# Optimization experiments

Hardware: AMD Instinct MI355X
Metric: run time of the kernel (lower is better)

Reference implementation:

```python
import jax, jax.numpy as jnp
import numpy as np

N = 100000   # nodes ('paper')
E = 500000   # edges per etype
ET = 3       # edge types
L = 2        # GAT layers
F = 256      # in_feats == h_feats
H = 4        # heads
D = 64       # head dim = h_feats // n_heads
C = 349      # num_classes
NEG_SLOPE = 0.2


def setup_inputs() -> dict:
    key = jax.random.key(0)
    ks = jax.random.split(key, 10)
    x = jax.random.normal(ks[0], (N, F), jnp.float32)
    # stacked per-(layer, etype) GATConv params
    W = jax.random.normal(ks[1], (L, ET, F, H * D), jnp.float32) * 0.05
    attn_l = jax.random.normal(ks[2], (L, ET, H, D), jnp.float32) * 0.1
    attn_r = jax.random.normal(ks[3], (L, ET, H, D), jnp.float32) * 0.1
    bias = jnp.zeros((L, ET, H * D), jnp.float32)
    W_out = jax.random.normal(ks[4], (H * D, C), jnp.float32) * 0.05
    b_out = jnp.zeros((C,), jnp.float32)
    src = jax.random.randint(ks[5], (ET, E), 0, N, dtype=jnp.int32)
    dst = jax.random.randint(ks[6], (ET, E), 0, N, dtype=jnp.int32)
    return {"x": x, "W": W, "attn_l": attn_l, "attn_r": attn_r, "bias": bias,
            "W_out": W_out, "b_out": b_out, "src": src, "dst": dst}


def _gat_etype(h, W_le, al, ar, b, s, d):
    # h: [N,F] -> feat: [N,H,D]
    feat = (h @ W_le).reshape(-1, H, D)
    el = jnp.einsum('nhd,hd->nh', feat, al)   # [N,H]
    er = jnp.einsum('nhd,hd->nh', feat, ar)   # [N,H]
    logits = jax.nn.leaky_relu(el[s] + er[d], NEG_SLOPE)  # [E,H]
    # segment softmax over incoming edges of each dst node
    m = jax.ops.segment_max(logits, d, num_segments=N)     # [N,H]
    a = jnp.exp(logits - m[d])                              # [E,H]
    denom = jax.ops.segment_sum(a, d, num_segments=N)      # [N,H]
    alpha = a / denom[d]                                    # [E,H]
    msg = alpha[:, :, None] * feat[s]                       # [E,H,D]
    agg = jax.ops.segment_sum(msg, d, num_segments=N)      # [N,H,D]
    return agg + b.reshape(H, D)


def reference(x, W, attn_l, attn_r, bias, W_out, b_out, src, dst):
    h = x
    for l in range(L):
        out = jnp.zeros((N, H, D), x.dtype)
        for e in range(ET):  # HeteroGraphConv default 'sum' aggregation
            out = out + _gat_etype(h, W[l, e], attn_l[l, e], attn_r[l, e],
                                   bias[l, e], src[e], dst[e])
        h = out.reshape(N, H * D)  # concat heads (view)
        if l != L - 1:
            h = jax.nn.relu(h)  # dropout is identity in eval mode
    return h @ W_out + b_out
```

## Files before the change

kernel.cpp:

```cpp
#include <hip/hip_runtime.h>
#include <hip/hip_fp16.h>

#define N_NODES 100000
#define N_EDGES 500000
#define M_PAD   100096
#define NCHUNK  196

using f32x4  = __attribute__((ext_vector_type(4))) float;
using bf16x8 = __attribute__((ext_vector_type(8))) __bf16;

__device__ __forceinline__ ushort f2bf(float f) {
  union { float f; unsigned u; } v; v.f = f;
  unsigned r = v.u + 0x7fffu + ((v.u >> 16) & 1u);
  return (ushort)(r >> 16);
}
__device__ __forceinline__ float bf2f(ushort b) {
  union { unsigned u; float f; } v; v.u = ((unsigned)b) << 16;
  return v.f;
}

__global__ __launch_bounds__(256) void cvt_x_kernel(const float* __restrict__ x,
                                                    ushort* __restrict__ h) {
  const size_t i = (size_t)blockIdx.x * 256 + threadIdx.x;
  ushort4 o;
  if (i < (size_t)N_NODES * 64) {
    const float4 v = ((const float4*)x)[i];
    o.x = f2bf(v.x); o.y = f2bf(v.y); o.z = f2bf(v.z); o.w = f2bf(v.w);
  } else {
    o.x = 0; o.y = 0; o.z = 0; o.w = 0;
  }
  ((ushort4*)h)[i] = o;
}

__global__ __launch_bounds__(256) void cvt_w_kernel(const float* __restrict__ W,
                                                    ushort* __restrict__ Wt) {
  const int i = blockIdx.x * 256 + threadIdx.x;
  const int le = i >> 16, r = i & 65535, nn = r >> 8, kk = r & 255;
  Wt[i] = f2bf(W[(le << 16) | (kk << 8) | nn]);
}

__global__ __launch_bounds__(256) void cvt_wout_kernel(const float* __restrict__ Wo,
                                                       ushort* __restrict__ Wto) {
  const int i = blockIdx.x * 256 + threadIdx.x;
  const int nn = i >> 8, kk = i & 255;
  Wto[i] = f2bf(nn < 349 ? Wo[kk * 349 + nn] : 0.f);
}

__global__ __launch_bounds__(256) void zero_cnt_kernel(int* __restrict__ cnt) {
  const int i = blockIdx.x * 256 + threadIdx.x;
  if (i < 3 * N_NODES) cnt[i] = 0;
}

__global__ __launch_bounds__(256) void hist_kernel(const int* __restrict__ dst,
                                                   int* __restrict__ cnt) {
  const int i = blockIdx.x * 256 + threadIdx.x;
  if (i >= 3 * N_EDGES) return;
  const int et = i / N_EDGES;
  atomicAdd(&cnt[et * N_NODES + dst[i]], 1);
}

__global__ __launch_bounds__(512) void scan1_kernel(const int* __restrict__ cnt,
                                                    int* __restrict__ rowp,
                                                    int* __restrict__ bsum) {
  __shared__ int sm[512];
  const int et = blockIdx.y, c = blockIdx.x, tid = threadIdx.x;
  const int idx = c * 512 + tid;
  const int v = (idx < N_NODES) ? cnt[et * N_NODES + idx] : 0;
  sm[tid] = v; __syncthreads();
  for (int off = 1; off < 512; off <<= 1) {
    const int tmp = (tid >= off) ? sm[tid - off] : 0;
    __syncthreads();
    sm[tid] += tmp;
    __syncthreads();
  }
  if (idx < N_NODES) rowp[et * (N_NODES + 1) + idx] = sm[tid] - v;
  if (tid == 511) bsum[et * NCHUNK + c] = sm[511];
}

__global__ __launch_bounds__(256) void scan2_kernel(int* __restrict__ bsum) {
  __shared__ int sm[256];
  const int et = blockIdx.x, tid = threadIdx.x;
  const int v = (tid < NCHUNK) ? bsum[et * NCHUNK + tid] : 0;
  sm[tid] = v; __syncthreads();
  for (int off = 1; off < 256; off <<= 1) {
    const int tmp = (tid >= off) ? sm[tid - off] : 0;
    __syncthreads();
    sm[tid] += tmp;
    __syncthreads();
  }
  if (tid < NCHUNK) bsum[et * NCHUNK + tid] = sm[tid] - v;
}

__global__ __launch_bounds__(512) void scan3_kernel(int* __restrict__ rowp,
                                                    const int* __restrict__ bsum,
                                                    int* __restrict__ cur) {
  const int et = blockIdx.y, c = blockIdx.x, tid = threadIdx.x;
  const int idx = c * 512 + tid;
  if (idx < N_NODES) {
    const int v = rowp[et * (N_NODES + 1) + idx] + bsum[et * NCHUNK + c];
    rowp[et * (N_NODES + 1) + idx] = v;
    cur[et * N_NODES + idx] = v;
  }
  if (c == 0 && tid == 0) rowp[et * (N_NODES + 1) + N_NODES] = N_EDGES;
}

__global__ __launch_bounds__(256) void scatter_kernel(const int* __restrict__ src,
                                                      const int* __restrict__ dst,
                                                      int* __restrict__ cur,
                                                      int* __restrict__ perm,
                                                      int* __restrict__ dstc) {
  const int i = blockIdx.x * 256 + threadIdx.x;
  if (i >= 3 * N_EDGES) return;
  const int et = i / N_EDGES;
  const int d = dst[i];
  const int pos = atomicAdd(&cur[et * N_NODES + d], 1);
  perm[et * N_EDGES + pos] = src[i];
  dstc[et * N_EDGES + pos] = d;
}

__global__ __launch_bounds__(256, 2) void gemm_feat_fused(
    const ushort* __restrict__ A, const ushort* __restrict__ WtL,
    ushort* __restrict__ feat, const float* __restrict__ attn_l,
    const float* __restrict__ attn_r, float* __restrict__ el,
    float* __restrict__ er, int layer) {
  __shared__ ushort As[128 * 64];
  __shared__ ushort Bs[3 * 128 * 64];
  const int t = threadIdx.x;
  const int lane = t & 63;
  const int wave = t >> 6;
  const int wm = (wave >> 1) << 6;
  const int wn = (wave & 1) << 6;
  const int quad = lane >> 4;
  const int ln = lane & 15;
  const size_t m0 = (size_t)blockIdx.x * 128;
  const size_t n0 = (size_t)blockIdx.y * 128;

  f32x4 acc[3][4][4];
#pragma unroll
  for (int e = 0; e < 3; ++e)
#pragma unroll
    for (int x = 0; x < 4; ++x)
#pragma unroll
      for (int y = 0; y < 4; ++y)
        acc[e][x][y] = (f32x4){0.f, 0.f, 0.f, 0.f};

  for (int k0 = 0; k0 < 256; k0 += 64) {
    __syncthreads();
#pragma unroll
    for (int i = 0; i < 4; ++i) {
      const int f = i * 256 + t;
      const int row = f >> 3;
      const int cl = (f & 7) ^ (row & 7);
      const int ldsbase = (i * 256 + (t & ~63)) << 3;
      __builtin_amdgcn_global_load_lds(
          (const __attribute__((address_space(1))) void*)(A + (m0 + row) * 256 + k0 + cl * 8),
          (__attribute__((address_space(3))) void*)(As + ldsbase), 16, 0, 0);
#pragma unroll
      for (int e = 0; e < 3; ++e)
        __builtin_amdgcn_global_load_lds(
            (const __attribute__((address_space(1))) void*)(WtL + (e << 16) + (n0 + row) * 256 + k0 + cl * 8),
            (__attribute__((address_space(3))) void*)(Bs + e * 8192 + ldsbase), 16, 0, 0);
    }
    __syncthreads();
#pragma unroll
    for (int s = 0; s < 2; ++s) {
      const int cl = s * 4 + quad;
      bf16x8 af[4];
#pragma unroll
      for (int x = 0; x < 4; ++x) {
        const int mm = wm + x * 16 + ln;
        af[x] = *(const bf16x8*)(As + mm * 64 + ((cl ^ (mm & 7)) << 3));
      }
#pragma unroll
      for (int e = 0; e < 3; ++e) {
        bf16x8 bfr[4];
#pragma unroll
        for (int y = 0; y < 4; ++y) {
          const int nn = wn + y * 16 + ln;
          bfr[y] = *(const bf16x8*)(Bs + e * 8192 + nn * 64 + ((cl ^ (nn & 7)) << 3));
        }
#pragma unroll
        for (int x = 0; x < 4; ++x)
#pragma unroll
          for (int y = 0; y < 4; ++y)
            acc[e][x][y] = __builtin_amdgcn_mfma_f32_16x16x32_bf16(bfr[y], af[x], acc[e][x][y], 0, 0, 0);
      }
    }
  }

  const int h = (int)(n0 + wn) >> 6;
#pragma unroll
  for (int e = 0; e < 3; ++e) {
    ushort* C = feat + (size_t)e * M_PAD * 256;
#pragma unroll
    for (int x = 0; x < 4; ++x) {
      const size_t m = m0 + wm + x * 16 + ln;
#pragma unroll
      for (int y = 0; y < 4; ++y) {
        const size_t n = n0 + wn + y * 16 + quad * 4;
        ushort4 o;
        o.x = f2bf(acc[e][x][y][0]); o.y = f2bf(acc[e][x][y][1]);
        o.z = f2bf(acc[e][x][y][2]); o.w = f2bf(acc[e][x][y][3]);
        *(ushort4*)(C + m * 256 + n) = o;
      }
    }
    const float* al = attn_l + (((layer * 3 + e) * 4 + h) << 6);
    const float* ar = attn_r + (((layer * 3 + e) * 4 + h) << 6);
    float4 alv[4], arv[4];
#pragma unroll
    for (int y = 0; y < 4; ++y) {
      alv[y] = *(const float4*)(al + y * 16 + quad * 4);
      arv[y] = *(const float4*)(ar + y * 16 + quad * 4);
    }
#pragma unroll
    for (int x = 0; x < 4; ++x) {
      float pl = 0.f, pr = 0.f;
#pragma unroll
      for (int y = 0; y < 4; ++y) {
        pl += acc[e][x][y][0] * alv[y].x + acc[e][x][y][1] * alv[y].y +
              acc[e][x][y][2] * alv[y].z + acc[e][x][y][3] * alv[y].w;
        pr += acc[e][x][y][0] * arv[y].x + acc[e][x][y][1] * arv[y].y +
              acc[e][x][y][2] * arv[y].z + acc[e][x][y][3] * arv[y].w;
      }
      pl += __shfl_xor(pl, 16); pl += __shfl_xor(pl, 32);
      pr += __shfl_xor(pr, 16); pr += __shfl_xor(pr, 32);
      const int m = (int)m0 + wm + x * 16 + ln;
      if (quad == 0 && m < N_NODES) {
        el[((size_t)e * N_NODES + m) * 4 + h] = pl;
        er[((size_t)e * N_NODES + m) * 4 + h] = pr;
      }
    }
  }
}

__global__ __launch_bounds__(256) void gemm128(const ushort* __restrict__ A,
                                               const ushort* __restrict__ Bt,
                                               float* __restrict__ C,
                                               const float* __restrict__ obias,
                                               int ldc, int nmax, int mmax) {
  __shared__ ushort As[128 * 64];
  __shared__ ushort Bs[128 * 64];
  const int t = threadIdx.x;
  const int lane = t & 63;
  const int wave = t >> 6;
  const int wm = (wave >> 1) << 6;
  const int wn = (wave & 1) << 6;
  const int quad = lane >> 4;
  const int ln = lane & 15;
  const size_t m0 = (size_t)blockIdx.x * 128;
  const size_t n0 = (size_t)blockIdx.y * 128;

  f32x4 acc[4][4];
#pragma unroll
  for (int x = 0; x < 4; ++x)
#pragma unroll
    for (int y = 0; y < 4; ++y)
      acc[x][y] = (f32x4){0.f, 0.f, 0.f, 0.f};

  for (int k0 = 0; k0 < 256; k0 += 64) {
    __syncthreads();
#pragma unroll
    for (int i = 0; i < 4; ++i) {
      const int f = i * 256 + t;
      const int row = f >> 3;
      const int cl = (f & 7) ^ (row & 7);
      const int ldsbase = (i * 256 + (t & ~63)) << 3;
      __builtin_amdgcn_global_load_lds(
          (const __attribute__((address_space(1))) void*)(A + (m0 + row) * 256 + k0 + cl * 8),
          (__attribute__((address_space(3))) void*)(As + ldsbase), 16, 0, 0);
      __builtin_amdgcn_global_load_lds(
          (const __attribute__((address_space(1))) void*)(Bt + (n0 + row) * 256 + k0 + cl * 8),
          (__attribute__((address_space(3))) void*)(Bs + ldsbase), 16, 0, 0);
    }
    __syncthreads();
#pragma unroll
    for (int s = 0; s < 2; ++s) {
      bf16x8 af[4], bfr[4];
      const int cl = s * 4 + quad;
#pragma unroll
      for (int x = 0; x < 4; ++x) {
        const int mm = wm + x * 16 + ln;
        af[x] = *(const bf16x8*)(As + mm * 64 + ((cl ^ (mm & 7)) << 3));
        const int nn = wn + x * 16 + ln;
        bfr[x] = *(const bf16x8*)(Bs + nn * 64 + ((cl ^ (nn & 7)) << 3));
      }
#pragma unroll
      for (int x = 0; x < 4; ++x)
#pragma unroll
        for (int y = 0; y < 4; ++y)
          acc[x][y] = __builtin_amdgcn_mfma_f32_16x16x32_bf16(bfr[y], af[x], acc[x][y], 0, 0, 0);
    }
  }

#pragma unroll
  for (int x = 0; x < 4; ++x) {
    const int m = (int)m0 + wm + x * 16 + ln;
    if (m < mmax) {
#pragma unroll
      for (int y = 0; y < 4; ++y) {
        const int n = (int)n0 + wn + y * 16 + quad * 4;
#pragma unroll
        for (int r = 0; r < 4; ++r)
          if (n + r < nmax)
            C[(size_t)m * ldc + n + r] = acc[x][y][r] + obias[n + r];
      }
    }
  }
}

__global__ __launch_bounds__(256) void wcalc_kernel(const int* __restrict__ perm,
                                                    const int* __restrict__ dstc,
                                                    const float* __restrict__ el,
                                                    const float* __restrict__ er,
                                                    ushort* __restrict__ wcsr) {
  const int i = blockIdx.x * 256 + threadIdx.x;
  if (i >= 3 * N_EDGES) return;
  const int et = i / N_EDGES;
  const int s = perm[i];
  const int d = dstc[i];
  const float4 l4 = ((const float4*)el)[(size_t)et * N_NODES + s];
  const float4 r4 = ((const float4*)er)[(size_t)et * N_NODES + d];
  float z0 = l4.x + r4.x, z1 = l4.y + r4.y, z2 = l4.z + r4.z, z3 = l4.w + r4.w;
  z0 = (z0 > 0.f) ? z0 : 0.2f * z0;
  z1 = (z1 > 0.f) ? z1 : 0.2f * z1;
  z2 = (z2 > 0.f) ? z2 : 0.2f * z2;
  z3 = (z3 > 0.f) ? z3 : 0.2f * z3;
  ushort4 o;
  o.x = __half_as_ushort(__float2half(__expf(z0)));
  o.y = __half_as_ushort(__float2half(__expf(z1)));
  o.z = __half_as_ushort(__float2half(__expf(z2)));
  o.w = __half_as_ushort(__float2half(__expf(z3)));
  ((ushort4*)wcsr)[i] = o;
}

__global__ __launch_bounds__(256) void agg_kernel(const ushort* __restrict__ feat,
                                                  const ushort* __restrict__ wcsr,
                                                  const int* __restrict__ rowp,
                                                  const int* __restrict__ perm,
                                                  const float* __restrict__ bias,
                                                  ushort* __restrict__ hout,
                                                  int layer, int do_relu) {
  const int wave = threadIdx.x >> 6, lane = threadIdx.x & 63;
  const int n = blockIdx.x * 4 + wave;
  const int h = lane >> 4;
  const float* bl = bias + layer * 768 + (lane << 2);
  float a0 = bl[0] + bl[256] + bl[512];
  float a1 = bl[1] + bl[257] + bl[513];
  float a2 = bl[2] + bl[258] + bl[514];
  float a3 = bl[3] + bl[259] + bl[515];
#pragma unroll
  for (int et = 0; et < 3; ++et) {
    const int beg = rowp[et * (N_NODES + 1) + n];
    const int end = rowp[et * (N_NODES + 1) + n + 1];
    if (end == beg) continue;
    const int* ps = perm + (size_t)et * N_EDGES;
    const ushort* wc = wcsr + (size_t)et * N_EDGES * 4;
    const ushort* fb = feat + (size_t)et * M_PAD * 256;
    const int last = end - 1;
    float l0 = 0.f, l1 = 0.f, l2 = 0.f, l3 = 0.f, den = 0.f;
    for (int i = beg; i < end; i += 8) {
      int idx[8];
#pragma unroll
      for (int j = 0; j < 8; ++j)
        idx[j] = (i + j < last) ? (i + j) : last;
      int sj[8];
#pragma unroll
      for (int j = 0; j < 8; ++j)
        sj[j] = ps[idx[j]];
      float wj[8];
#pragma unroll
      for (int j = 0; j < 8; ++j) {
        const float t = __half2float(__ushort_as_half(wc[idx[j] * 4 + h]));
        wj[j] = (i + j <= last) ? t : 0.f;
      }
      ushort4 fv[8];
#pragma unroll
      for (int j = 0; j < 8; ++j)
        fv[j] = *(const ushort4*)(fb + (size_t)sj[j] * 256 + (lane << 2));
#pragma unroll
      for (int j = 0; j < 8; ++j) {
        den += wj[j];
        l0 += wj[j] * bf2f(fv[j].x); l1 += wj[j] * bf2f(fv[j].y);
        l2 += wj[j] * bf2f(fv[j].z); l3 += wj[j] * bf2f(fv[j].w);
      }
    }
    const float inv = 1.0f / den;
    a0 += l0 * inv; a1 += l1 * inv; a2 += l2 * inv; a3 += l3 * inv;
  }
  if (do_relu) {
    a0 = fmaxf(a0, 0.f); a1 = fmaxf(a1, 0.f);
    a2 = fmaxf(a2, 0.f); a3 = fmaxf(a3, 0.f);
  }
  ushort4 o;
  o.x = f2bf(a0); o.y = f2bf(a1); o.z = f2bf(a2); o.w = f2bf(a3);
  *(ushort4*)(hout + (size_t)n * 256 + (lane << 2)) = o;
}

extern "C" void kernel_launch(void* const* d_in, const int* in_sizes, int n_in,
                              void* d_out, int out_size, void* d_ws, size_t ws_size,
                              hipStream_t stream) {
  const float* x      = (const float*)d_in[0];
  const float* W      = (const float*)d_in[1];
  const float* attn_l = (const float*)d_in[2];
  const float* attn_r = (const float*)d_in[3];
  const float* bias   = (const float*)d_in[4];
  const float* W_out  = (const float*)d_in[5];
  const float* b_out  = (const float*)d_in[6];
  const int*   src    = (const int*)d_in[7];
  const int*   dst    = (const int*)d_in[8];

  char* p = (char*)d_ws;
  auto carve = [&](size_t bytes) {
    char* r = p;
    p += (bytes + 255) & ~(size_t)255;
    return r;
  };
  ushort* h_bf  = (ushort*)carve((size_t)M_PAD * 256 * 2);
  ushort* feat  = (ushort*)carve((size_t)3 * M_PAD * 256 * 2);
  ushort* Wt    = (ushort*)carve((size_t)6 * 65536 * 2);
  ushort* Wto   = (ushort*)carve((size_t)384 * 256 * 2);
  float*  el    = (float*)carve((size_t)3 * N_NODES * 4 * 4);
  float*  er    = (float*)carve((size_t)3 * N_NODES * 4 * 4);
  int*    cnt   = (int*)carve((size_t)3 * N_NODES * 4);
  int*    rowp  = (int*)carve((size_t)3 * (N_NODES + 1) * 4);
  int*    cur   = (int*)carve((size_t)3 * N_NODES * 4);
  int*    perm  = (int*)carve((size_t)3 * N_EDGES * 4);
  int*    dstc  = (int*)carve((size_t)3 * N_EDGES * 4);
  ushort* wcsr  = (ushort*)carve((size_t)3 * N_EDGES * 4 * 2);
  int*    bsum  = (int*)carve((size_t)3 * NCHUNK * 4);

  cvt_x_kernel<<<M_PAD * 64 / 256, 256, 0, stream>>>(x, h_bf);
  cvt_w_kernel<<<6 * 65536 / 256, 256, 0, stream>>>(W, Wt);
  cvt_wout_kernel<<<384 * 256 / 256, 256, 0, stream>>>(W_out, Wto);

  zero_cnt_kernel<<<(3 * N_NODES + 255) / 256, 256, 0, stream>>>(cnt);
  hist_kernel<<<(3 * N_EDGES + 255) / 256, 256, 0, stream>>>(dst, cnt);
  scan1_kernel<<<dim3(NCHUNK, 3), 512, 0, stream>>>(cnt, rowp, bsum);
  scan2_kernel<<<3, 256, 0, stream>>>(bsum);
  scan3_kernel<<<dim3(NCHUNK, 3), 512, 0, stream>>>(rowp, bsum, cur);
  scatter_kernel<<<(3 * N_EDGES + 255) / 256, 256, 0, stream>>>(src, dst, cur, perm, dstc);

  for (int l = 0; l < 2; ++l) {
    gemm_feat_fused<<<dim3(M_PAD / 128, 2), 256, 0, stream>>>(
        h_bf, Wt + (size_t)l * 3 * 65536, feat, attn_l, attn_r, el, er, l);
    wcalc_kernel<<<(3 * N_EDGES + 255) / 256, 256, 0, stream>>>(perm, dstc, el, er, wcsr);
    agg_kernel<<<N_NODES / 4, 256, 0, stream>>>(feat, wcsr, rowp, perm, bias,
                                                h_bf, l, l == 0 ? 1 : 0);
  }
  gemm128<<<dim3(M_PAD / 128, 3), 256, 0, stream>>>(h_bf, Wto, (float*)d_out,
                                                    b_out, 349, 349, N_NODES);
}
```

Measured before the change: 980.8 us.

## Merge per-etype CSRs into one dst CSR with prenormalized attention weights

Builds a single CSR over all three edge types keyed by destination. Each edge stores global src/dst ids offset by etype*M_PAD. Softmax denominators are computed by atomic adds in wcalc, inverted, and folded into the fp16 weights by a new normalization pass, so aggregation visits each node's edges in one loop with no per-etype divide. The aggregation kernel also becomes a grid-stride loop over 2048 blocks. This adds several extra kernels and float atomics per layer, and normalizing in fp16 changes rounding.

```diff
diff --git a/kernel.cpp b/kernel.cpp
--- a/kernel.cpp
+++ b/kernel.cpp
@@ -5,6 +5,7 @@
 #define N_EDGES 500000
 #define M_PAD   100096
 #define NCHUNK  196
+#define DEN_ELEMS (3 * M_PAD * 4)
 
 using f32x4  = __attribute__((ext_vector_type(4))) float;
 using bf16x8 = __attribute__((ext_vector_type(8))) __bf16;
@@ -48,24 +49,23 @@
 
 __global__ __launch_bounds__(256) void zero_cnt_kernel(int* __restrict__ cnt) {
   const int i = blockIdx.x * 256 + threadIdx.x;
-  if (i < 3 * N_NODES) cnt[i] = 0;
+  if (i < N_NODES) cnt[i] = 0;
 }
 
 __global__ __launch_bounds__(256) void hist_kernel(const int* __restrict__ dst,
                                                    int* __restrict__ cnt) {
   const int i = blockIdx.x * 256 + threadIdx.x;
   if (i >= 3 * N_EDGES) return;
-  const int et = i / N_EDGES;
-  atomicAdd(&cnt[et * N_NODES + dst[i]], 1);
+  atomicAdd(&cnt[dst[i]], 1);
 }
 
 __global__ __launch_bounds__(512) void scan1_kernel(const int* __restrict__ cnt,
                                                     int* __restrict__ rowp,
                                                     int* __restrict__ bsum) {
   __shared__ int sm[512];
-  const int et = blockIdx.y, c = blockIdx.x, tid = threadIdx.x;
+  const int c = blockIdx.x, tid = threadIdx.x;
   const int idx = c * 512 + tid;
-  const int v = (idx < N_NODES) ? cnt[et * N_NODES + idx] : 0;
+  const int v = (idx < N_NODES) ? cnt[idx] : 0;
   sm[tid] = v; __syncthreads();
   for (int off = 1; off < 512; off <<= 1) {
     const int tmp = (tid >= off) ? sm[tid - off] : 0;
@@ -73,14 +73,14 @@
     sm[tid] += tmp;
     __syncthreads();
   }
-  if (idx < N_NODES) rowp[et * (N_NODES + 1) + idx] = sm[tid] - v;
-  if (tid == 511) bsum[et * NCHUNK + c] = sm[511];
+  if (idx < N_NODES) rowp[idx] = sm[tid] - v;
+  if (tid == 511) bsum[c] = sm[511];
 }
 
 __global__ __launch_bounds__(256) void scan2_kernel(int* __restrict__ bsum) {
   __shared__ int sm[256];
-  const int et = blockIdx.x, tid = threadIdx.x;
-  const int v = (tid < NCHUNK) ? bsum[et * NCHUNK + tid] : 0;
+  const int tid = threadIdx.x;
+  const int v = (tid < NCHUNK) ? bsum[tid] : 0;
   sm[tid] = v; __syncthreads();
   for (int off = 1; off < 256; off <<= 1) {
     const int tmp = (tid >= off) ? sm[tid - off] : 0;
@@ -88,34 +88,34 @@
     sm[tid] += tmp;
     __syncthreads();
   }
-  if (tid < NCHUNK) bsum[et * NCHUNK + tid] = sm[tid] - v;
+  if (tid < NCHUNK) bsum[tid] = sm[tid] - v;
 }
 
 __global__ __launch_bounds__(512) void scan3_kernel(int* __restrict__ rowp,
                                                     const int* __restrict__ bsum,
                                                     int* __restrict__ cur) {
-  const int et = blockIdx.y, c = blockIdx.x, tid = threadIdx.x;
+  const int c = blockIdx.x, tid = threadIdx.x;
   const int idx = c * 512 + tid;
   if (idx < N_NODES) {
-    const int v = rowp[et * (N_NODES + 1) + idx] + bsum[et * NCHUNK + c];
-    rowp[et * (N_NODES + 1) + idx] = v;
-    cur[et * N_NODES + idx] = v;
-  }
-  if (c == 0 && tid == 0) rowp[et * (N_NODES + 1) + N_NODES] = N_EDGES;
+    const int v = rowp[idx] + bsum[c];
+    rowp[idx] = v;
+    cur[idx] = v;
+  }
+  if (c == 0 && tid == 0) rowp[N_NODES] = 3 * N_EDGES;
 }
 
 __global__ __launch_bounds__(256) void scatter_kernel(const int* __restrict__ src,
                                                       const int* __restrict__ dst,
                                                       int* __restrict__ cur,
-                                                      int* __restrict__ perm,
-                                                      int* __restrict__ dstc) {
+                                                      uint* __restrict__ srcid,
+                                                      uint* __restrict__ dstid) {
   const int i = blockIdx.x * 256 + threadIdx.x;
   if (i >= 3 * N_EDGES) return;
   const int et = i / N_EDGES;
   const int d = dst[i];
-  const int pos = atomicAdd(&cur[et * N_NODES + d], 1);
-  perm[et * N_EDGES + pos] = src[i];
-  dstc[et * N_EDGES + pos] = d;
+  const int pos = atomicAdd(&cur[d], 1);
+  srcid[pos] = (uint)(et * M_PAD + src[i]);
+  dstid[pos] = (uint)(et * M_PAD + d);
 }
 
 __global__ __launch_bounds__(256, 2) void gemm_feat_fused(
@@ -226,8 +226,8 @@
       pr += __shfl_xor(pr, 16); pr += __shfl_xor(pr, 32);
       const int m = (int)m0 + wm + x * 16 + ln;
       if (quad == 0 && m < N_NODES) {
-        el[((size_t)e * N_NODES + m) * 4 + h] = pl;
-        er[((size_t)e * N_NODES + m) * 4 + h] = pr;
+        el[((size_t)e * M_PAD + m) * 4 + h] = pl;
+        er[((size_t)e * M_PAD + m) * 4 + h] = pr;
       }
     }
   }
@@ -308,92 +308,132 @@
   }
 }
 
-__global__ __launch_bounds__(256) void wcalc_kernel(const int* __restrict__ perm,
-                                                    const int* __restrict__ dstc,
+__global__ __launch_bounds__(256) void wcalc_kernel(const uint* __restrict__ srcid,
+                                                    const uint* __restrict__ dstid,
                                                     const float* __restrict__ el,
                                                     const float* __restrict__ er,
-                                                    ushort* __restrict__ wcsr) {
+                                                    ushort* __restrict__ wcsr,
+                                                    float* __restrict__ den) {
   const int i = blockIdx.x * 256 + threadIdx.x;
   if (i >= 3 * N_EDGES) return;
-  const int et = i / N_EDGES;
-  const int s = perm[i];
-  const int d = dstc[i];
-  const float4 l4 = ((const float4*)el)[(size_t)et * N_NODES + s];
-  const float4 r4 = ((const float4*)er)[(size_t)et * N_NODES + d];
+  const uint sid = srcid[i];
+  const uint did = dstid[i];
+  const float4 l4 = ((const float4*)el)[sid];
+  const float4 r4 = ((const float4*)er)[did];
   float z0 = l4.x + r4.x, z1 = l4.y + r4.y, z2 = l4.z + r4.z, z3 = l4.w + r4.w;
   z0 = (z0 > 0.f) ? z0 : 0.2f * z0;
   z1 = (z1 > 0.f) ? z1 : 0.2f * z1;
   z2 = (z2 > 0.f) ? z2 : 0.2f * z2;
   z3 = (z3 > 0.f) ? z3 : 0.2f * z3;
+  const float w0 = __expf(z0), w1 = __expf(z1), w2 = __expf(z2), w3 = __expf(z3);
   ushort4 o;
-  o.x = __half_as_ushort(__float2half(__expf(z0)));
-  o.y = __half_as_ushort(__float2half(__expf(z1)));
-  o.z = __half_as_ushort(__float2half(__expf(z2)));
-  o.w = __half_as_ushort(__float2half(__expf(z3)));
+  o.x = __half_as_ushort(__float2half(w0));
+  o.y = __half_as_ushort(__float2half(w1));
+  o.z = __half_as_ushort(__float2half(w2));
+  o.w = __half_as_ushort(__float2half(w3));
+  ((ushort4*)wcsr)[i] = o;
+  float* dp = den + (size_t)did * 4;
+  atomicAdd(dp + 0, w0); atomicAdd(dp + 1, w1);
+  atomicAdd(dp + 2, w2); atomicAdd(dp + 3, w3);
+}
+
+__global__ __launch_bounds__(256) void zero_den_kernel(float* __restrict__ den) {
+  const int i = blockIdx.x * 256 + threadIdx.x;
+  if (i < DEN_ELEMS) den[i] = 0.f;
+}
+
+__global__ __launch_bounds__(256) void rcp_den_kernel(float* __restrict__ den) {
+  const int i = blockIdx.x * 256 + threadIdx.x;
+  if (i < DEN_ELEMS) {
+    const float d = den[i];
+    den[i] = (d != 0.f) ? __builtin_amdgcn_rcpf(d) : 0.f;
+  }
+}
+
+__global__ __launch_bounds__(256) void wnorm_kernel(const uint* __restrict__ dstid,
+                                                    const float* __restrict__ rden,
+                                                    ushort* __restrict__ wcsr) {
+  const int i = blockIdx.x * 256 + threadIdx.x;
+  if (i >= 3 * N_EDGES) return;
+  const uint did = dstid[i];
+  const float4 r4 = ((const float4*)rden)[did];
+  const ushort4 w = ((const ushort4*)wcsr)[i];
+  ushort4 o;
+  o.x = __half_as_ushort(__float2half(__half2float(__ushort_as_half(w.x)) * r4.x));
+  o.y = __half_as_ushort(__float2half(__half2float(__ushort_as_half(w.y)) * r4.y));
+  o.z = __half_as_ushort(__float2half(__half2float(__ushort_as_half(w.z)) * r4.z));
+  o.w = __half_as_ushort(__float2half(__half2float(__ushort_as_half(w.w)) * r4.w));
   ((ushort4*)wcsr)[i] = o;
 }
 
 __global__ __launch_bounds__(256) void agg_kernel(const ushort* __restrict__ feat,
                                                   const ushort* __restrict__ wcsr,
                                                   const int* __restrict__ rowp,
-                                                  const int* __restrict__ perm,
+                                                  const uint* __restrict__ srcid,
                                                   const float* __restrict__ bias,
                                                   ushort* __restrict__ hout,
                                                   int layer, int do_relu) {
-  const int wave = threadIdx.x >> 6, lane = threadIdx.x & 63;
-  const int n = blockIdx.x * 4 + wave;
-  const int h = lane >> 4;
+  const int wv   = __builtin_amdgcn_readfirstlane((int)(threadIdx.x >> 6));
+  const int lane = threadIdx.x & 63;
+  const int h2   = (lane >> 4) << 1;
+  const int f8   = lane << 3;
   const float* bl = bias + layer * 768 + (lane << 2);
-  float a0 = bl[0] + bl[256] + bl[512];
-  float a1 = bl[1] + bl[257] + bl[513];
-  float a2 = bl[2] + bl[258] + bl[514];
-  float a3 = bl[3] + bl[259] + bl[515];
-#pragma unroll
-  for (int et = 0; et < 3; ++et) {
-    const int beg = rowp[et * (N_NODES + 1) + n];
-    const int end = rowp[et * (N_NODES + 1) + n + 1];
-    if (end == beg) continue;
-    const int* ps = perm + (size_t)et * N_EDGES;
-    const ushort* wc = wcsr + (size_t)et * N_EDGES * 4;
-    const ushort* fb = feat + (size_t)et * M_PAD * 256;
-    const int last = end - 1;
-    float l0 = 0.f, l1 = 0.f, l2 = 0.f, l3 = 0.f, den = 0.f;
-    for (int i = beg; i < end; i += 8) {
-      int idx[8];
-#pragma unroll
-      for (int j = 0; j < 8; ++j)
-        idx[j] = (i + j < last) ? (i + j) : last;
-      int sj[8];
-#pragma unroll
-      for (int j = 0; j < 8; ++j)
-        sj[j] = ps[idx[j]];
-      float wj[8];
-#pragma unroll
-      for (int j = 0; j < 8; ++j) {
-        const float t = __half2float(__ushort_as_half(wc[idx[j] * 4 + h]));
-        wj[j] = (i + j <= last) ? t : 0.f;
-      }
-      ushort4 fv[8];
-#pragma unroll
-      for (int j = 0; j < 8; ++j)
-        fv[j] = *(const ushort4*)(fb + (size_t)sj[j] * 256 + (lane << 2));
-#pragma unroll
-      for (int j = 0; j < 8; ++j) {
-        den += wj[j];
-        l0 += wj[j] * bf2f(fv[j].x); l1 += wj[j] * bf2f(fv[j].y);
-        l2 += wj[j] * bf2f(fv[j].z); l3 += wj[j] * bf2f(fv[j].w);
-      }
-    }
-    const float inv = 1.0f / den;
-    a0 += l0 * inv; a1 += l1 * inv; a2 += l2 * inv; a3 += l3 * inv;
-  }
-  if (do_relu) {
-    a0 = fmaxf(a0, 0.f); a1 = fmaxf(a1, 0.f);
-    a2 = fmaxf(a2, 0.f); a3 = fmaxf(a3, 0.f);
-  }
-  ushort4 o;
-  o.x = f2bf(a0); o.y = f2bf(a1); o.z = f2bf(a2); o.w = f2bf(a3);
-  *(ushort4*)(hout + (size_t)n * 256 + (lane << 2)) = o;
+  const float b0 = bl[0] + bl[256] + bl[512];
+  const float b1 = bl[1] + bl[257] + bl[513];
+  const float b2 = bl[2] + bl[258] + bl[514];
+  const float b3 = bl[3] + bl[259] + bl[515];
+  const char* wb = (const char*)wcsr;
+  const char* fb = (const char*)feat;
+  for (int n = blockIdx.x * 4 + wv; n < N_NODES; n += 8192) {
+    const int beg = rowp[n];
+    const int end = rowp[n + 1];
+    float a0 = b0, a1 = b1, a2 = b2, a3 = b3;
+    if (end > beg) {
+      const int last = end - 1;
+      float l0 = 0.f, l1 = 0.f, l2 = 0.f, l3 = 0.f;
+      for (int i = beg; i < end; i += 8) {
+        int idx[8];
+#pragma unroll
+        for (int j = 0; j < 8; ++j)
+          idx[j] = (i + j < last) ? (i + j) : last;
+        uint sd[8];
+#pragma unroll
+        for (int j = 0; j < 8; ++j)
+          sd[j] = srcid[idx[j]];
+        float wj[8];
+#pragma unroll
+        for (int j = 0; j < 8; ++j) {
+          const ushort wu = *(const ushort*)(wb + ((size_t)idx[j] << 3) + h2);
+          const float t = __half2float(__ushort_as_half(wu));
+          wj[j] = (i + j <= last) ? t : 0.f;
+        }
+        uint2 fv[8];
+#pragma unroll
+        for (int j = 0; j < 8; ++j)
+          fv[j] = *(const uint2*)(fb + ((size_t)sd[j] << 9) + f8);
+#pragma unroll
+        for (int j = 0; j < 8; ++j) {
+          union { uint u; float f; } c0, c1, c2, c3;
+          c0.u = fv[j].x << 16;
+          c1.u = fv[j].x & 0xffff0000u;
+          c2.u = fv[j].y << 16;
+          c3.u = fv[j].y & 0xffff0000u;
+          l0 += wj[j] * c0.f;
+          l1 += wj[j] * c1.f;
+          l2 += wj[j] * c2.f;
+          l3 += wj[j] * c3.f;
+        }
+      }
+      a0 += l0; a1 += l1; a2 += l2; a3 += l3;
+    }
+    if (do_relu) {
+      a0 = fmaxf(a0, 0.f); a1 = fmaxf(a1, 0.f);
+      a2 = fmaxf(a2, 0.f); a3 = fmaxf(a3, 0.f);
+    }
+    ushort4 o;
+    o.x = f2bf(a0); o.y = f2bf(a1); o.z = f2bf(a2); o.w = f2bf(a3);
+    *(ushort4*)(hout + (size_t)n * 256 + (lane << 2)) = o;
+  }
 }
 
 extern "C" void kernel_launch(void* const* d_in, const int* in_sizes, int n_in,
@@ -419,33 +459,37 @@
   ushort* feat  = (ushort*)carve((size_t)3 * M_PAD * 256 * 2);
   ushort* Wt    = (ushort*)carve((size_t)6 * 65536 * 2);
   ushort* Wto   = (ushort*)carve((size_t)384 * 256 * 2);
-  float*  el    = (float*)carve((size_t)3 * N_NODES * 4 * 4);
-  float*  er    = (float*)carve((size_t)3 * N_NODES * 4 * 4);
-  int*    cnt   = (int*)carve((size_t)3 * N_NODES * 4);
-  int*    rowp  = (int*)carve((size_t)3 * (N_NODES + 1) * 4);
-  int*    cur   = (int*)carve((size_t)3 * N_NODES * 4);
-  int*    perm  = (int*)carve((size_t)3 * N_EDGES * 4);
-  int*    dstc  = (int*)carve((size_t)3 * N_EDGES * 4);
+  float*  el    = (float*)carve((size_t)3 * M_PAD * 4 * 4);
+  float*  er    = (float*)carve((size_t)3 * M_PAD * 4 * 4);
+  float*  den   = (float*)carve((size_t)DEN_ELEMS * 4);
+  int*    cnt   = (int*)carve((size_t)N_NODES * 4);
+  int*    rowp  = (int*)carve((size_t)(N_NODES + 1) * 4);
+  int*    cur   = (int*)carve((size_t)N_NODES * 4);
+  uint*   srcid = (uint*)carve((size_t)3 * N_EDGES * 4);
+  uint*   dstid = (uint*)carve((size_t)3 * N_EDGES * 4);
   ushort* wcsr  = (ushort*)carve((size_t)3 * N_EDGES * 4 * 2);
-  int*    bsum  = (int*)carve((size_t)3 * NCHUNK * 4);
+  int*    bsum  = (int*)carve((size_t)NCHUNK * 4);
 
   cvt_x_kernel<<<M_PAD * 64 / 256, 256, 0, stream>>>(x, h_bf);
   cvt_w_kernel<<<6 * 65536 / 256, 256, 0, stream>>>(W, Wt);
   cvt_wout_kernel<<<384 * 256 / 256, 256, 0, stream>>>(W_out, Wto);
 
-  zero_cnt_kernel<<<(3 * N_NODES + 255) / 256, 256, 0, stream>>>(cnt);
+  zero_cnt_kernel<<<(N_NODES + 255) / 256, 256, 0, stream>>>(cnt);
   hist_kernel<<<(3 * N_EDGES + 255) / 256, 256, 0, stream>>>(dst, cnt);
-  scan1_kernel<<<dim3(NCHUNK, 3), 512, 0, stream>>>(cnt, rowp, bsum);
-  scan2_kernel<<<3, 256, 0, stream>>>(bsum);
-  scan3_kernel<<<dim3(NCHUNK, 3), 512, 0, stream>>>(rowp, bsum, cur);
-  scatter_kernel<<<(3 * N_EDGES + 255) / 256, 256, 0, stream>>>(src, dst, cur, perm, dstc);
+  scan1_kernel<<<NCHUNK, 512, 0, stream>>>(cnt, rowp, bsum);
+  scan2_kernel<<<1, 256, 0, stream>>>(bsum);
+  scan3_kernel<<<NCHUNK, 512, 0, stream>>>(rowp, bsum, cur);
+  scatter_kernel<<<(3 * N_EDGES + 255) / 256, 256, 0, stream>>>(src, dst, cur, srcid, dstid);
 
   for (int l = 0; l < 2; ++l) {
     gemm_feat_fused<<<dim3(M_PAD / 128, 2), 256, 0, stream>>>(
         h_bf, Wt + (size_t)l * 3 * 65536, feat, attn_l, attn_r, el, er, l);
-    wcalc_kernel<<<(3 * N_EDGES + 255) / 256, 256, 0, stream>>>(perm, dstc, el, er, wcsr);
-    agg_kernel<<<N_NODES / 4, 256, 0, stream>>>(feat, wcsr, rowp, perm, bias,
-                                                h_bf, l, l == 0 ? 1 : 0);
+    zero_den_kernel<<<(DEN_ELEMS + 255) / 256, 256, 0, stream>>>(den);
+    wcalc_kernel<<<(3 * N_EDGES + 255) / 256, 256, 0, stream>>>(srcid, dstid, el, er, wcsr, den);
+    rcp_den_kernel<<<(DEN_ELEMS + 255) / 256, 256, 0, stream>>>(den);
+    wnorm_kernel<<<(3 * N_EDGES + 255) / 256, 256, 0, stream>>>(dstid, den, wcsr);
+    agg_kernel<<<2048, 256, 0, stream>>>(feat, wcsr, rowp, srcid, bias,
+                                         h_bf, l, l == 0 ? 1 : 0);
   }
   gemm128<<<dim3(M_PAD / 128, 3), 256, 0, stream>>>(h_bf, Wto, (float*)d_out,
                                                     b_out, 349, 349, N_NODES);
```

Measured after the change: 1.515 ms. 1.54x slower.
